# Performance work log

Measured on AMD Instinct MI355X. Metric: run time of the kernel, lower is better.

## Reference

```python
import jax, jax.numpy as jnp
import numpy as np

S, B, DIM = 1024, 4, 768
N_EXPERTS = 8
# hidden_dim = 256 * ceil(int(2*4*dim/3)/256) = 2048 for dim=768
HID = 2048


def setup_inputs() -> dict:
    key = jax.random.key(0)
    ks = jax.random.split(key, 6)
    scale = 0.02
    return {
        "hidden_states": jax.random.normal(ks[0], (S, B, DIM), dtype=jnp.float32),
        "router_w": jax.random.normal(ks[1], (DIM, N_EXPERTS), dtype=jnp.float32) * scale,
        "router_b": jnp.zeros((N_EXPERTS,), dtype=jnp.float32),
        "w1": jax.random.normal(ks[2], (N_EXPERTS, DIM, HID), dtype=jnp.float32) * scale,
        "w2": jax.random.normal(ks[3], (N_EXPERTS, DIM, HID), dtype=jnp.float32) * scale,
        "w3": jax.random.normal(ks[4], (N_EXPERTS, HID, DIM), dtype=jnp.float32) * scale,
    }


def reference(hidden_states, router_w, router_b, w1, w2, w3):
    s, b, h = hidden_states.shape
    # top-1 router
    route = jax.nn.softmax(hidden_states @ router_w + router_b, axis=2)  # [s,b,E]
    max_prob = jnp.max(route, axis=2).reshape(-1, 1)   # [T,1]
    max_ind = jnp.argmax(route, axis=2).reshape(-1)    # [T]
    x = hidden_states.reshape(-1, h)                   # [T,d]

    out = jnp.zeros_like(x)
    # fixed small loop over experts; masked dispatch (tokens not routed to e
    # are zeroed so they contribute nothing)
    for e in range(N_EXPERTS):
        mask = (max_ind == e)[:, None]                 # [T,1]
        xe = jnp.where(mask, x, 0.0)
        oe = (jax.nn.silu(xe @ w1[e]) * (xe @ w2[e])) @ w3[e]
        out = out + jnp.where(mask, oe, 0.0)

    # original stores expert outputs in a bf16 buffer before the prob combine
    out = out.astype(jnp.bfloat16) * max_prob          # bf16 * f32 -> f32
    return out.reshape(s, b, h)
```

## Files before the change

### kernel.cpp

```cpp
#include <hip/hip_runtime.h>


#define T_TOK 4096
#define DIM   768
#define HID   2048
#define NE    8
#define ECAP  1024

#define KB1 (DIM / 32)
#define NB1 (HID / 16)
#define KB2 (HID / 32)
#define NB2 (DIM / 16)
#define MBC (ECAP / 16)

typedef _Float16 f16x8 __attribute__((ext_vector_type(8)));
typedef _Float16 f16x4 __attribute__((ext_vector_type(4)));
typedef float    f32x4 __attribute__((ext_vector_type(4)));

__device__ __forceinline__ float bf16_rne(float v) {
    unsigned u = __float_as_uint(v);
    unsigned r = (u + 0x7fffu + ((u >> 16) & 1u)) & 0xffff0000u;
    return __uint_as_float(r);
}

__global__ void moe_init_kernel(int* __restrict__ counts) {
    if (threadIdx.x < NE) counts[threadIdx.x] = 0;
}

__global__ __launch_bounds__(256) void moe_convert_kernel(
    const float* __restrict__ w1, const float* __restrict__ w2,
    const float* __restrict__ w3, _Float16* __restrict__ w1s,
    _Float16* __restrict__ w2s, _Float16* __restrict__ w3s)
{
    const int z = blockIdx.z, e = z & 7, mat = z >> 3;
    const float* src; _Float16* dst; int K, N;
    if (mat == 0)      { src = w1 + (size_t)e * DIM * HID; dst = w1s + (size_t)e * NB1 * KB1 * 512; K = DIM; N = HID; }
    else if (mat == 1) { src = w2 + (size_t)e * DIM * HID; dst = w2s + (size_t)e * NB1 * KB1 * 512; K = DIM; N = HID; }
    else               { src = w3 + (size_t)e * HID * DIM; dst = w3s + (size_t)e * NB2 * KB2 * 512; K = HID; N = DIM; }
    const int ngrp = blockIdx.x, kb = blockIdx.y;
    if (ngrp * 128 >= N || kb * 32 >= K) return;
    const int KBc = K >> 5;

    __shared__ _Float16 Lt[128 * 40];
    const int t  = threadIdx.x;
    const int n4 = (t & 31) * 4;
    const int k4 = (t >> 5) * 4;
    const float* p = src + (size_t)(kb * 32 + k4) * N + ngrp * 128 + n4;
    float4 v[4];
#pragma unroll
    for (int j = 0; j < 4; ++j) v[j] = *(const float4*)(p + (size_t)j * N);
#pragma unroll
    for (int i = 0; i < 4; ++i) {
        f16x4 q;
#pragma unroll
        for (int j = 0; j < 4; ++j) q[j] = (_Float16)(((const float*)&v[j])[i]);
        *(f16x4*)&Lt[(n4 + i) * 40 + k4] = q;
    }
    __syncthreads();
    const int w = t >> 6, l = t & 63;
#pragma unroll
    for (int c = 0; c < 2; ++c) {
        const int nbl = w * 2 + c;
        f16x8 fr = *(const f16x8*)&Lt[(nbl * 16 + (l & 15)) * 40 + (l >> 4) * 8];
        const int nb = ngrp * 8 + nbl;
        *(f16x8*)(dst + ((size_t)nb * KBc + kb) * 512 + l * 8) = fr;
    }
}

__global__ __launch_bounds__(256) void moe_router_kernel(
    const float* __restrict__ X, const float* __restrict__ rw,
    const float* __restrict__ rb, float* __restrict__ probs,
    int* __restrict__ counts, int* __restrict__ lists)
{
    const int t    = blockIdx.x * 4 + (threadIdx.x >> 6);
    const int lane = threadIdx.x & 63;
    const float* x = X + (size_t)t * DIM;

    float xv[12];
#pragma unroll
    for (int j = 0; j < 12; ++j) xv[j] = x[lane + j * 64];

    double lg[NE];
#pragma unroll
    for (int e = 0; e < NE; ++e) {
        double s = 0.0;
#pragma unroll
        for (int j = 0; j < 12; ++j)
            s += (double)xv[j] * (double)rw[(lane + j * 64) * NE + e];
#pragma unroll
        for (int off = 32; off >= 1; off >>= 1) s += __shfl_xor(s, off, 64);
        lg[e] = s + (double)rb[e];
    }

    if (lane == 0) {
        double m = lg[0]; int mi = 0;
#pragma unroll
        for (int e = 1; e < NE; ++e)
            if (lg[e] > m) { m = lg[e]; mi = e; }
        float sum = 0.f;
#pragma unroll
        for (int e = 0; e < NE; ++e) sum += expf((float)(lg[e] - m));
        probs[t] = 1.0f / sum;
        int pos = atomicAdd(&counts[mi], 1);
        lists[mi * T_TOK + pos] = t;
    }
}

__global__ __launch_bounds__(256) void moe_gather_kernel(
    const float* __restrict__ X, const int* __restrict__ lists,
    const int* __restrict__ counts, _Float16* __restrict__ Ag)
{
    const int e = blockIdx.z;
    int cnt = counts[e]; if (cnt > ECAP) cnt = ECAP;
    const int mgrp = blockIdx.y;
    if (mgrp * 64 >= ((cnt + 63) & ~63)) return;
    const int t = threadIdx.x, w = t >> 6, l = t & 63;
    const int mb = mgrp * 4 + w;
    const int m  = mb * 16 + (l & 15);
    const bool valid = (m < cnt);
    const int tok = valid ? lists[e * T_TOK + m] : 0;
    const float* xr = X + (size_t)tok * DIM + (l >> 4) * 8;
#pragma unroll
    for (int i = 0; i < 4; ++i) {
        const int kb = blockIdx.x * 4 + i;
        float4 a = make_float4(0.f, 0.f, 0.f, 0.f), b = a;
        if (valid) {
            a = *(const float4*)(xr + kb * 32);
            b = *(const float4*)(xr + kb * 32 + 4);
        }
        f16x8 h;
        h[0] = (_Float16)a.x; h[1] = (_Float16)a.y; h[2] = (_Float16)a.z; h[3] = (_Float16)a.w;
        h[4] = (_Float16)b.x; h[5] = (_Float16)b.y; h[6] = (_Float16)b.z; h[7] = (_Float16)b.w;
        *(f16x8*)(Ag + ((size_t)(e * MBC + mb) * KB1 + kb) * 512 + l * 8) = h;
    }
}

__global__ __launch_bounds__(256) void moe_gemm1_kernel(
    const _Float16* __restrict__ Ag, const _Float16* __restrict__ w1s,
    const _Float16* __restrict__ w2s, const int* __restrict__ counts,
    _Float16* __restrict__ Hs)
{
    const int e = blockIdx.z;
    int cnt = counts[e]; if (cnt > ECAP) cnt = ECAP;
    const int by = blockIdx.y, bx = blockIdx.x;
    if (by * 64 >= cnt) return;
    const int t = threadIdx.x, w = t >> 6, l = t & 63;

    const _Float16* Ab  = Ag  + ((size_t)(e * MBC + by * 4) * KB1) * 512 + l * 8;
    const int nb0 = bx * 8 + w * 2;
    const _Float16* B1b = w1s + ((size_t)(e * NB1 + nb0) * KB1) * 512 + l * 8;
    const _Float16* B2b = w2s + ((size_t)(e * NB1 + nb0) * KB1) * 512 + l * 8;

    f32x4 acc1[4][2], acc2[4][2];
    const f32x4 zero = {0.f, 0.f, 0.f, 0.f};
#pragma unroll
    for (int i = 0; i < 4; ++i)
#pragma unroll
        for (int j = 0; j < 2; ++j) { acc1[i][j] = zero; acc2[i][j] = zero; }

#pragma unroll 2
    for (int kb = 0; kb < KB1; ++kb) {
        f16x8 a[4], b1[2], b2[2];
#pragma unroll
        for (int i = 0; i < 4; ++i)
            a[i] = *(const f16x8*)(Ab + (i * KB1 + kb) * 512);
#pragma unroll
        for (int j = 0; j < 2; ++j) {
            b1[j] = *(const f16x8*)(B1b + (j * KB1 + kb) * 512);
            b2[j] = *(const f16x8*)(B2b + (j * KB1 + kb) * 512);
        }
#pragma unroll
        for (int i = 0; i < 4; ++i)
#pragma unroll
            for (int j = 0; j < 2; ++j) {
                acc1[i][j] = __builtin_amdgcn_mfma_f32_16x16x32_f16(a[i], b1[j], acc1[i][j], 0, 0, 0);
                acc2[i][j] = __builtin_amdgcn_mfma_f32_16x16x32_f16(a[i], b2[j], acc2[i][j], 0, 0, 0);
            }
    }

    __shared__ _Float16 Ep[4][64 * 40];
    const int fq = l >> 4, fr = l & 15;
#pragma unroll
    for (int i = 0; i < 4; ++i)
#pragma unroll
        for (int j = 0; j < 2; ++j)
#pragma unroll
            for (int r = 0; r < 4; ++r) {
                const float h1 = acc1[i][j][r], h2 = acc2[i][j][r];
                const float s  = h1 / (1.f + __expf(-h1)) * h2;
                Ep[w][(i * 16 + fq * 4 + r) * 40 + j * 16 + fr] = (_Float16)s;
            }
    __syncthreads();
    const int kbH = bx * 4 + w;
#pragma unroll
    for (int i = 0; i < 4; ++i) {
        f16x8 v = *(const f16x8*)&Ep[w][(i * 16 + fr) * 40 + fq * 8];
        *(f16x8*)(Hs + ((size_t)(e * MBC + by * 4 + i) * KB2 + kbH) * 512 + l * 8) = v;
    }
}

__global__ __launch_bounds__(256) void moe_gemm2_kernel(
    const _Float16* __restrict__ Hs, const _Float16* __restrict__ w3s,
    const int* __restrict__ lists, const int* __restrict__ counts,
    const float* __restrict__ probs, float* __restrict__ out)
{
    const int e = blockIdx.z;
    int cnt = counts[e]; if (cnt > ECAP) cnt = ECAP;
    const int by = blockIdx.y, bx = blockIdx.x;
    const int m0 = by * 32;
    if (m0 >= cnt) return;
    const int t = threadIdx.x, w = t >> 6, l = t & 63;

    const _Float16* Ab = Hs  + ((size_t)(e * MBC + by * 2) * KB2) * 512 + l * 8;
    const int nb0 = bx * 8 + w * 2;
    const _Float16* Bb = w3s + ((size_t)(e * NB2 + nb0) * KB2) * 512 + l * 8;

    f32x4 acc[2][2];
    const f32x4 zero = {0.f, 0.f, 0.f, 0.f};
    acc[0][0] = zero; acc[0][1] = zero; acc[1][0] = zero; acc[1][1] = zero;

#pragma unroll 4
    for (int kb = 0; kb < KB2; ++kb) {
        f16x8 a[2], b[2];
#pragma unroll
        for (int i = 0; i < 2; ++i)
            a[i] = *(const f16x8*)(Ab + (i * KB2 + kb) * 512);
#pragma unroll
        for (int j = 0; j < 2; ++j)
            b[j] = *(const f16x8*)(Bb + (j * KB2 + kb) * 512);
#pragma unroll
        for (int i = 0; i < 2; ++i)
#pragma unroll
            for (int j = 0; j < 2; ++j)
                acc[i][j] = __builtin_amdgcn_mfma_f32_16x16x32_f16(a[i], b[j], acc[i][j], 0, 0, 0);
    }

    const int* list = lists + e * T_TOK;
    const int fq = l >> 4, fr = l & 15;
    const int c0 = bx * 128 + w * 32;
#pragma unroll
    for (int i = 0; i < 2; ++i)
#pragma unroll
        for (int r = 0; r < 4; ++r) {
            const int m = m0 + i * 16 + fq * 4 + r;
            if (m < cnt) {
                const int tok = list[m];
                const float pb = probs[tok];
                float* orow = out + (size_t)tok * DIM + c0 + fr;
                orow[0]  = bf16_rne(acc[i][0][r]) * pb;
                orow[16] = bf16_rne(acc[i][1][r]) * pb;
            }
        }
}

extern "C" void kernel_launch(void* const* d_in, const int* in_sizes, int n_in,
                              void* d_out, int out_size, void* d_ws, size_t ws_size,
                              hipStream_t stream) {
    const float* X  = (const float*)d_in[0];
    const float* rw = (const float*)d_in[1];
    const float* rb = (const float*)d_in[2];
    const float* w1 = (const float*)d_in[3];
    const float* w2 = (const float*)d_in[4];
    const float* w3 = (const float*)d_in[5];
    float* out = (float*)d_out;

    char* ws = (char*)d_ws;
    int*      counts = (int*)(ws + 0);
    int*      lists  = (int*)(ws + 256);
    float*    probs  = (float*)(ws + 131328);
    const size_t WSZ = 25165824;
    _Float16* w1s = (_Float16*)(ws + 147712);
    _Float16* w2s = (_Float16*)(ws + 147712 + WSZ);
    _Float16* w3s = (_Float16*)(ws + 147712 + 2 * WSZ);
    _Float16* Ag  = (_Float16*)(ws + 147712 + 3 * WSZ);
    _Float16* Hs  = (_Float16*)(ws + 147712 + 3 * WSZ + 12582912);

    hipLaunchKernelGGL(moe_init_kernel, dim3(1), dim3(64), 0, stream, counts);
    hipLaunchKernelGGL(moe_convert_kernel, dim3(16, 64, 24), dim3(256), 0, stream,
                       w1, w2, w3, w1s, w2s, w3s);
    hipLaunchKernelGGL(moe_router_kernel, dim3(T_TOK / 4), dim3(256), 0, stream,
                       X, rw, rb, probs, counts, lists);
    hipLaunchKernelGGL(moe_gather_kernel, dim3(6, 16, 8), dim3(256), 0, stream,
                       X, lists, counts, Ag);
    hipLaunchKernelGGL(moe_gemm1_kernel, dim3(16, 16, 8), dim3(256), 0, stream,
                       Ag, w1s, w2s, counts, Hs);
    hipLaunchKernelGGL(moe_gemm2_kernel, dim3(6, 32, 8), dim3(256), 0, stream,
                       Hs, w3s, lists, counts, probs, out);
}
```

Baseline: 349.2 us.

## Fuse weight conversion with router, split list building, remap GEMM blocks per XCD

Weight conversion and router logits now run in one prep kernel, and the separate init kernel is gone. The conversion reads columns with strided scalar loads and no LDS transpose. The router uses vectorized float4 loads and writes an expert id per token. A small lists kernel then builds the per-expert token lists with atomics, capped at ECAP. The GEMM kernels use a flat grid with an XCD-aware block mapping so blocks sharing an expert's weight columns land on the same XCD for L2 reuse. The risks are uncoalesced strided reads in the conversion and one extra launch for the lists.

```diff
diff --git a/kernel.cpp b/kernel.cpp
--- a/kernel.cpp
+++ b/kernel.cpp
@@ -6,15 +6,14 @@
 #define HID   2048
 #define NE    8
 #define ECAP  1024
-
-#define KB1 (DIM / 32)
-#define NB1 (HID / 16)
-#define KB2 (HID / 32)
-#define NB2 (DIM / 16)
-#define MBC (ECAP / 16)
+#define KB1   24
+#define NB1   128
+#define KB2   64
+#define NB2   48
+#define MBC   64
+#define ESTRIDE 1572864
 
 typedef _Float16 f16x8 __attribute__((ext_vector_type(8)));
-typedef _Float16 f16x4 __attribute__((ext_vector_type(4)));
 typedef float    f32x4 __attribute__((ext_vector_type(4)));
 
 __device__ __forceinline__ float bf16_rne(float v) {
@@ -23,87 +22,98 @@
     return __uint_as_float(r);
 }
 
-__global__ void moe_init_kernel(int* __restrict__ counts) {
-    if (threadIdx.x < NE) counts[threadIdx.x] = 0;
-}
-
-__global__ __launch_bounds__(256) void moe_convert_kernel(
+__global__ __launch_bounds__(256) void moe_prep_kernel(
     const float* __restrict__ w1, const float* __restrict__ w2,
-    const float* __restrict__ w3, _Float16* __restrict__ w1s,
-    _Float16* __restrict__ w2s, _Float16* __restrict__ w3s)
-{
-    const int z = blockIdx.z, e = z & 7, mat = z >> 3;
-    const float* src; _Float16* dst; int K, N;
-    if (mat == 0)      { src = w1 + (size_t)e * DIM * HID; dst = w1s + (size_t)e * NB1 * KB1 * 512; K = DIM; N = HID; }
-    else if (mat == 1) { src = w2 + (size_t)e * DIM * HID; dst = w2s + (size_t)e * NB1 * KB1 * 512; K = DIM; N = HID; }
-    else               { src = w3 + (size_t)e * HID * DIM; dst = w3s + (size_t)e * NB2 * KB2 * 512; K = HID; N = DIM; }
-    const int ngrp = blockIdx.x, kb = blockIdx.y;
-    if (ngrp * 128 >= N || kb * 32 >= K) return;
-    const int KBc = K >> 5;
-
-    __shared__ _Float16 Lt[128 * 40];
-    const int t  = threadIdx.x;
-    const int n4 = (t & 31) * 4;
-    const int k4 = (t >> 5) * 4;
-    const float* p = src + (size_t)(kb * 32 + k4) * N + ngrp * 128 + n4;
-    float4 v[4];
-#pragma unroll
-    for (int j = 0; j < 4; ++j) v[j] = *(const float4*)(p + (size_t)j * N);
-#pragma unroll
-    for (int i = 0; i < 4; ++i) {
-        f16x4 q;
-#pragma unroll
-        for (int j = 0; j < 4; ++j) q[j] = (_Float16)(((const float*)&v[j])[i]);
-        *(f16x4*)&Lt[(n4 + i) * 40 + k4] = q;
-    }
-    __syncthreads();
-    const int w = t >> 6, l = t & 63;
-#pragma unroll
-    for (int c = 0; c < 2; ++c) {
-        const int nbl = w * 2 + c;
-        f16x8 fr = *(const f16x8*)&Lt[(nbl * 16 + (l & 15)) * 40 + (l >> 4) * 8];
-        const int nb = ngrp * 8 + nbl;
-        *(f16x8*)(dst + ((size_t)nb * KBc + kb) * 512 + l * 8) = fr;
-    }
-}
-
-__global__ __launch_bounds__(256) void moe_router_kernel(
-    const float* __restrict__ X, const float* __restrict__ rw,
-    const float* __restrict__ rb, float* __restrict__ probs,
-    int* __restrict__ counts, int* __restrict__ lists)
-{
-    const int t    = blockIdx.x * 4 + (threadIdx.x >> 6);
-    const int lane = threadIdx.x & 63;
-    const float* x = X + (size_t)t * DIM;
-
-    float xv[12];
-#pragma unroll
-    for (int j = 0; j < 12; ++j) xv[j] = x[lane + j * 64];
-
-    double lg[NE];
-#pragma unroll
-    for (int e = 0; e < NE; ++e) {
-        double s = 0.0;
-#pragma unroll
-        for (int j = 0; j < 12; ++j)
-            s += (double)xv[j] * (double)rw[(lane + j * 64) * NE + e];
-#pragma unroll
-        for (int off = 32; off >= 1; off >>= 1) s += __shfl_xor(s, off, 64);
-        lg[e] = s + (double)rb[e];
-    }
-
-    if (lane == 0) {
-        double m = lg[0]; int mi = 0;
-#pragma unroll
-        for (int e = 1; e < NE; ++e)
-            if (lg[e] > m) { m = lg[e]; mi = e; }
-        float sum = 0.f;
-#pragma unroll
-        for (int e = 0; e < NE; ++e) sum += expf((float)(lg[e] - m));
-        probs[t] = 1.0f / sum;
-        int pos = atomicAdd(&counts[mi], 1);
-        lists[mi * T_TOK + pos] = t;
-    }
+    const float* __restrict__ w3, const float* __restrict__ X,
+    const float* __restrict__ rw, const float* __restrict__ rb,
+    _Float16* __restrict__ w1s, _Float16* __restrict__ w2s,
+    _Float16* __restrict__ w3s, int* __restrict__ eid,
+    float* __restrict__ probs, int* __restrict__ counts)
+{
+    const int bid = blockIdx.x;
+    const int t = threadIdx.x, w = t >> 6, l = t & 63;
+    if (bid < 1152) {
+        if (bid == 0 && t < NE) counts[t] = 0;
+        const int mat = bid / 384;
+        const float* src = (mat == 0) ? w1 : (mat == 1) ? w2 : w3;
+        _Float16*    dst = (mat == 0) ? w1s : (mat == 1) ? w2s : w3s;
+        const int N   = (mat == 2) ? DIM : HID;
+        const int KBc = (mat == 2) ? KB2 : KB1;
+        const int fq = l >> 4, fr = l & 15;
+        const int cbase = (bid % 384) * 64 + w * 16;
+#pragma unroll
+        for (int ch = 0; ch < 4; ++ch) {
+            const int cid = cbase + ch * 4;
+            const int e   = cid / 3072;
+            const int r   = cid - e * 3072;
+            const int nb  = r / KBc;
+            const int kb0 = r - nb * KBc;
+            const float* sp = src + (size_t)e * ESTRIDE
+                            + (size_t)(fq * 8) * N + nb * 16 + fr;
+            float v[4][8];
+#pragma unroll
+            for (int i = 0; i < 4; ++i)
+#pragma unroll
+                for (int j = 0; j < 8; ++j)
+                    v[i][j] = sp[(size_t)((kb0 + i) * 32 + j) * N];
+            _Float16* dp = dst + ((size_t)e * 3072 + (size_t)nb * KBc + kb0) * 512 + l * 8;
+#pragma unroll
+            for (int i = 0; i < 4; ++i) {
+                f16x8 h;
+#pragma unroll
+                for (int j = 0; j < 8; ++j) h[j] = (_Float16)v[i][j];
+                *(f16x8*)(dp + i * 512) = h;
+            }
+        }
+    } else {
+        const int tok = (bid - 1152) * 4 + w;
+        const float4* X4 = (const float4*)(X + (size_t)tok * DIM);
+        float4 xq[3];
+#pragma unroll
+        for (int jj = 0; jj < 3; ++jj) xq[jj] = X4[l + jj * 64];
+        double lg[NE] = {0, 0, 0, 0, 0, 0, 0, 0};
+#pragma unroll
+        for (int jj = 0; jj < 3; ++jj)
+#pragma unroll
+            for (int q = 0; q < 4; ++q) {
+                const int row = (l + jj * 64) * 4 + q;
+                const double xv = (double)((const float*)&xq[jj])[q];
+                const float4 w0 = *(const float4*)(rw + row * 8);
+                const float4 w1v = *(const float4*)(rw + row * 8 + 4);
+                lg[0] += xv * (double)w0.x;  lg[1] += xv * (double)w0.y;
+                lg[2] += xv * (double)w0.z;  lg[3] += xv * (double)w0.w;
+                lg[4] += xv * (double)w1v.x; lg[5] += xv * (double)w1v.y;
+                lg[6] += xv * (double)w1v.z; lg[7] += xv * (double)w1v.w;
+            }
+#pragma unroll
+        for (int e = 0; e < NE; ++e) {
+#pragma unroll
+            for (int off = 32; off >= 1; off >>= 1)
+                lg[e] += __shfl_xor(lg[e], off, 64);
+            lg[e] += (double)rb[e];
+        }
+        if (l == 0) {
+            double m = lg[0]; int mi = 0;
+#pragma unroll
+            for (int e = 1; e < NE; ++e)
+                if (lg[e] > m) { m = lg[e]; mi = e; }
+            float sum = 0.f;
+#pragma unroll
+            for (int e = 0; e < NE; ++e) sum += expf((float)(lg[e] - m));
+            probs[tok] = 1.0f / sum;
+            eid[tok] = mi;
+        }
+    }
+}
+
+__global__ __launch_bounds__(256) void moe_lists_kernel(
+    const int* __restrict__ eid, int* __restrict__ counts,
+    int* __restrict__ lists)
+{
+    const int t = blockIdx.x * 256 + threadIdx.x;
+    const int e = eid[t];
+    const int pos = atomicAdd(&counts[e], 1);
+    if (pos < ECAP) lists[e * ECAP + pos] = t;
 }
 
 __global__ __launch_bounds__(256) void moe_gather_kernel(
@@ -118,7 +128,7 @@
     const int mb = mgrp * 4 + w;
     const int m  = mb * 16 + (l & 15);
     const bool valid = (m < cnt);
-    const int tok = valid ? lists[e * T_TOK + m] : 0;
+    const int tok = valid ? lists[e * ECAP + m] : 0;
     const float* xr = X + (size_t)tok * DIM + (l >> 4) * 8;
 #pragma unroll
     for (int i = 0; i < 4; ++i) {
@@ -140,16 +150,19 @@
     const _Float16* __restrict__ w2s, const int* __restrict__ counts,
     _Float16* __restrict__ Hs)
 {
-    const int e = blockIdx.z;
+    const int b = blockIdx.x;
+    const int xcd = b & 7, slot = b >> 3;
+    const int mb = slot & 15, cgrp = slot >> 4;
+    const int c = cgrp * 8 + xcd;
+    const int e = c >> 4, nb = c & 15;
     int cnt = counts[e]; if (cnt > ECAP) cnt = ECAP;
-    const int by = blockIdx.y, bx = blockIdx.x;
-    if (by * 64 >= cnt) return;
+    if (mb * 64 >= cnt) return;
     const int t = threadIdx.x, w = t >> 6, l = t & 63;
 
-    const _Float16* Ab  = Ag  + ((size_t)(e * MBC + by * 4) * KB1) * 512 + l * 8;
-    const int nb0 = bx * 8 + w * 2;
-    const _Float16* B1b = w1s + ((size_t)(e * NB1 + nb0) * KB1) * 512 + l * 8;
-    const _Float16* B2b = w2s + ((size_t)(e * NB1 + nb0) * KB1) * 512 + l * 8;
+    const _Float16* Ab = Ag + ((size_t)(e * MBC + mb * 4) * KB1) * 512 + l * 8;
+    const int nc0 = e * NB1 + nb * 8 + w * 2;
+    const _Float16* B1b = w1s + ((size_t)nc0 * KB1) * 512 + l * 8;
+    const _Float16* B2b = w2s + ((size_t)nc0 * KB1) * 512 + l * 8;
 
     f32x4 acc1[4][2], acc2[4][2];
     const f32x4 zero = {0.f, 0.f, 0.f, 0.f};
@@ -160,21 +173,21 @@
 
 #pragma unroll 2
     for (int kb = 0; kb < KB1; ++kb) {
-        f16x8 a[4], b1[2], b2[2];
+        f16x8 a[4], p[2], q[2];
 #pragma unroll
         for (int i = 0; i < 4; ++i)
-            a[i] = *(const f16x8*)(Ab + (i * KB1 + kb) * 512);
+            a[i] = *(const f16x8*)(Ab + ((size_t)(i * KB1 + kb)) * 512);
 #pragma unroll
         for (int j = 0; j < 2; ++j) {
-            b1[j] = *(const f16x8*)(B1b + (j * KB1 + kb) * 512);
-            b2[j] = *(const f16x8*)(B2b + (j * KB1 + kb) * 512);
+            p[j] = *(const f16x8*)(B1b + ((size_t)(j * KB1 + kb)) * 512);
+            q[j] = *(const f16x8*)(B2b + ((size_t)(j * KB1 + kb)) * 512);
         }
 #pragma unroll
         for (int i = 0; i < 4; ++i)
 #pragma unroll
             for (int j = 0; j < 2; ++j) {
-                acc1[i][j] = __builtin_amdgcn_mfma_f32_16x16x32_f16(a[i], b1[j], acc1[i][j], 0, 0, 0);
-                acc2[i][j] = __builtin_amdgcn_mfma_f32_16x16x32_f16(a[i], b2[j], acc2[i][j], 0, 0, 0);
+                acc1[i][j] = __builtin_amdgcn_mfma_f32_16x16x32_f16(a[i], p[j], acc1[i][j], 0, 0, 0);
+                acc2[i][j] = __builtin_amdgcn_mfma_f32_16x16x32_f16(a[i], q[j], acc2[i][j], 0, 0, 0);
             }
     }
 
@@ -191,11 +204,11 @@
                 Ep[w][(i * 16 + fq * 4 + r) * 40 + j * 16 + fr] = (_Float16)s;
             }
     __syncthreads();
-    const int kbH = bx * 4 + w;
+    const int kbH = nb * 4 + w;
 #pragma unroll
     for (int i = 0; i < 4; ++i) {
         f16x8 v = *(const f16x8*)&Ep[w][(i * 16 + fr) * 40 + fq * 8];
-        *(f16x8*)(Hs + ((size_t)(e * MBC + by * 4 + i) * KB2 + kbH) * 512 + l * 8) = v;
+        *(f16x8*)(Hs + ((size_t)((e * MBC + mb * 4 + i) * KB2 + kbH)) * 512 + l * 8) = v;
     }
 }
 
@@ -204,16 +217,18 @@
     const int* __restrict__ lists, const int* __restrict__ counts,
     const float* __restrict__ probs, float* __restrict__ out)
 {
-    const int e = blockIdx.z;
+    const int b = blockIdx.x;
+    const int xcd = b & 7, slot = b >> 3;
+    const int mb = slot & 31, cgrp = slot >> 5;
+    const int c = cgrp * 8 + xcd;
+    const int e = c / 6, nb = c - e * 6;
     int cnt = counts[e]; if (cnt > ECAP) cnt = ECAP;
-    const int by = blockIdx.y, bx = blockIdx.x;
-    const int m0 = by * 32;
-    if (m0 >= cnt) return;
+    if (mb * 32 >= cnt) return;
     const int t = threadIdx.x, w = t >> 6, l = t & 63;
 
-    const _Float16* Ab = Hs  + ((size_t)(e * MBC + by * 2) * KB2) * 512 + l * 8;
-    const int nb0 = bx * 8 + w * 2;
-    const _Float16* Bb = w3s + ((size_t)(e * NB2 + nb0) * KB2) * 512 + l * 8;
+    const _Float16* Ab = Hs + ((size_t)((e * MBC + mb * 2) * KB2)) * 512 + l * 8;
+    const int nc0 = e * NB2 + nb * 8 + w * 2;
+    const _Float16* Bb = w3s + ((size_t)nc0 * KB2) * 512 + l * 8;
 
     f32x4 acc[2][2];
     const f32x4 zero = {0.f, 0.f, 0.f, 0.f};
@@ -221,28 +236,28 @@
 
 #pragma unroll 4
     for (int kb = 0; kb < KB2; ++kb) {
-        f16x8 a[2], b[2];
+        f16x8 a[2], bf[2];
 #pragma unroll
         for (int i = 0; i < 2; ++i)
-            a[i] = *(const f16x8*)(Ab + (i * KB2 + kb) * 512);
+            a[i] = *(const f16x8*)(Ab + ((size_t)(i * KB2 + kb)) * 512);
 #pragma unroll
         for (int j = 0; j < 2; ++j)
-            b[j] = *(const f16x8*)(Bb + (j * KB2 + kb) * 512);
+            bf[j] = *(const f16x8*)(Bb + ((size_t)(j * KB2 + kb)) * 512);
 #pragma unroll
         for (int i = 0; i < 2; ++i)
 #pragma unroll
             for (int j = 0; j < 2; ++j)
-                acc[i][j] = __builtin_amdgcn_mfma_f32_16x16x32_f16(a[i], b[j], acc[i][j], 0, 0, 0);
-    }
-
-    const int* list = lists + e * T_TOK;
+                acc[i][j] = __builtin_amdgcn_mfma_f32_16x16x32_f16(a[i], bf[j], acc[i][j], 0, 0, 0);
+    }
+
+    const int* list = lists + e * ECAP;
     const int fq = l >> 4, fr = l & 15;
-    const int c0 = bx * 128 + w * 32;
+    const int c0 = nb * 128 + w * 32;
 #pragma unroll
     for (int i = 0; i < 2; ++i)
 #pragma unroll
         for (int r = 0; r < 4; ++r) {
-            const int m = m0 + i * 16 + fq * 4 + r;
+            const int m = mb * 32 + i * 16 + fq * 4 + r;
             if (m < cnt) {
                 const int tok = list[m];
                 const float pb = probs[tok];
@@ -266,24 +281,24 @@
 
     char* ws = (char*)d_ws;
     int*      counts = (int*)(ws + 0);
-    int*      lists  = (int*)(ws + 256);
-    float*    probs  = (float*)(ws + 131328);
+    int*      eid    = (int*)(ws + 256);
+    float*    probs  = (float*)(ws + 16640);
+    int*      lists  = (int*)(ws + 33024);
     const size_t WSZ = 25165824;
-    _Float16* w1s = (_Float16*)(ws + 147712);
-    _Float16* w2s = (_Float16*)(ws + 147712 + WSZ);
-    _Float16* w3s = (_Float16*)(ws + 147712 + 2 * WSZ);
-    _Float16* Ag  = (_Float16*)(ws + 147712 + 3 * WSZ);
-    _Float16* Hs  = (_Float16*)(ws + 147712 + 3 * WSZ + 12582912);
-
-    hipLaunchKernelGGL(moe_init_kernel, dim3(1), dim3(64), 0, stream, counts);
-    hipLaunchKernelGGL(moe_convert_kernel, dim3(16, 64, 24), dim3(256), 0, stream,
-                       w1, w2, w3, w1s, w2s, w3s);
-    hipLaunchKernelGGL(moe_router_kernel, dim3(T_TOK / 4), dim3(256), 0, stream,
-                       X, rw, rb, probs, counts, lists);
+    _Float16* w1s = (_Float16*)(ws + 65792);
+    _Float16* w2s = (_Float16*)(ws + 65792 + WSZ);
+    _Float16* w3s = (_Float16*)(ws + 65792 + 2 * WSZ);
+    _Float16* Ag  = (_Float16*)(ws + 65792 + 3 * WSZ);
+    _Float16* Hs  = (_Float16*)(ws + 65792 + 3 * WSZ + 12582912);
+
+    hipLaunchKernelGGL(moe_prep_kernel, dim3(2176), dim3(256), 0, stream,
+                       w1, w2, w3, X, rw, rb, w1s, w2s, w3s, eid, probs, counts);
+    hipLaunchKernelGGL(moe_lists_kernel, dim3(16), dim3(256), 0, stream,
+                       eid, counts, lists);
     hipLaunchKernelGGL(moe_gather_kernel, dim3(6, 16, 8), dim3(256), 0, stream,
                        X, lists, counts, Ag);
-    hipLaunchKernelGGL(moe_gemm1_kernel, dim3(16, 16, 8), dim3(256), 0, stream,
+    hipLaunchKernelGGL(moe_gemm1_kernel, dim3(2048), dim3(256), 0, stream,
                        Ag, w1s, w2s, counts, Hs);
-    hipLaunchKernelGGL(moe_gemm2_kernel, dim3(6, 32, 8), dim3(256), 0, stream,
+    hipLaunchKernelGGL(moe_gemm2_kernel, dim3(1536), dim3(256), 0, stream,
                        Hs, w3s, lists, counts, probs, out);
 }
```

Result: no change. 349.8 us (+0.2%).
